# Kernel optimization log

Measured on AMD Instinct MI355X. Metric: run time of the kernel, lower is better.

The kernel has to match this reference:

```python
import jax, jax.numpy as jnp
import numpy as np


def conv3x3_reflect(x, w):
    # x: [B,C,H,W], w: [O,I,3,3]; reflect pad 1, stride 1, no bias
    xp = jnp.pad(x, ((0, 0), (0, 0), (1, 1), (1, 1)), mode='reflect')
    return jax.lax.conv_general_dilated(
        xp, w, window_strides=(1, 1), padding='VALID',
        dimension_numbers=('NCHW', 'OIHW', 'NCHW'))


def prelu(x, alpha):
    return jnp.where(x >= 0, x, alpha * x)


def nonlocal_block(x, wg, wth, wph, wW):
    # x: [B,C,H,W]; all weights [O,C] (1x1 convs, no bias)
    B, C, H, W = x.shape
    xf = x.reshape(B, C, H * W)                     # [B,C,N]
    g_x = jnp.einsum('oc,bcn->bno', wg, xf)         # [B,N,Ci]
    theta_x = jnp.einsum('oc,bcn->bno', wth, xf)    # [B,N,Ci]
    phi_x = jnp.einsum('oc,bcn->bon', wph, xf)      # [B,Ci,N]
    f = jnp.einsum('bic,bcj->bij', theta_x, phi_x)  # [B,N,N]
    # NOTE: original code softmaxes over dim=1 (rows), not the last dim
    f_div_C = jax.nn.softmax(f, axis=1)
    y = jnp.einsum('bij,bjc->bic', f_div_C, g_x)    # [B,N,Ci]
    y = y.transpose(0, 2, 1).reshape(B, -1, H, W)   # [B,Ci,H,W]
    W_y = jnp.einsum('oc,bchw->bohw', wW, y)
    return W_y + x


def setup_inputs() -> dict:
    key = jax.random.key(0)
    ks = jax.random.split(key, 8)
    B, C, H, W = 2, 64, 80, 80
    s33 = 1.0 / np.sqrt(C * 9)
    s11 = 1.0 / np.sqrt(C)
    return {
        'x': jax.random.normal(ks[0], (B, C, H, W), jnp.float32),
        'w1': jax.random.normal(ks[1], (C, C, 3, 3), jnp.float32) * s33,
        'w2': jax.random.normal(ks[2], (C, C, 3, 3), jnp.float32) * s33,
        'wg': jax.random.normal(ks[3], (C, C), jnp.float32) * s11,
        'wth': jax.random.normal(ks[4], (C, C), jnp.float32) * s11,
        'wph': jax.random.normal(ks[5], (C, C), jnp.float32) * s11,
        'wW': jax.random.normal(ks[6], (C, C), jnp.float32) * s11,
        'alpha': jnp.asarray(0.25, jnp.float32),
    }


def reference(x, w1, w2, wg, wth, wph, wW, alpha):
    x1 = conv3x3_reflect(x, w1)          # conv1; becomes residual source
    out = prelu(x1, alpha)
    out = nonlocal_block(out, wg, wth, wph, wW)
    out = out + x1                       # out += x (x was rebound to conv1 output)
    out = conv3x3_reflect(out, w2)       # conv2 (BasicConv, relu=False, bn=None)
    out = prelu(out, alpha)
    return out
```

## Files before the change

kernel.cpp:

```cpp
#include <hip/hip_runtime.h>
#include <hip/hip_bf16.h>
#include <cstddef>


constexpr int kB = 2, kC = 64, kH = 80, kW = 80, kN = kH * kW;
constexpr int kSJ = 10, kChunk = kN / kSJ, kNT = kChunk / 64;
constexpr float kLOG2E = 1.4426950408889634f;

typedef __attribute__((ext_vector_type(8))) short short8;
typedef __attribute__((ext_vector_type(4))) float f32x4;

__device__ __forceinline__ uint pkbf(float a, float b) {
  union { __hip_bfloat162 h; uint u; } x;
  x.h.x = __float2bfloat16(a);
  x.h.y = __float2bfloat16(b);
  return x.u;
}

__device__ __forceinline__ uint pktr(float a, float b) {
  return __builtin_amdgcn_perm(__float_as_uint(b), __float_as_uint(a),
                               0x07060302u);
}

#define GL16(gsrc, ldst)                                                    \
  __builtin_amdgcn_global_load_lds(                                         \
      (__attribute__((address_space(1))) void*)(char*)(gsrc),               \
      (__attribute__((address_space(3))) void*)(ldst), 16, 0, 0)

__global__ void k_prep(const float* __restrict__ w1, const float* __restrict__ w2,
                       const float* __restrict__ wth, const float* __restrict__ wph,
                       const float* __restrict__ wg, const float* __restrict__ wWm,
                       ushort* __restrict__ wc1, ushort* __restrict__ wc2,
                       __hip_bfloat16* __restrict__ Mb,
                       __hip_bfloat16* __restrict__ wgb,
                       __hip_bfloat16* __restrict__ wWb) {
  const int idx = blockIdx.x * 256 + threadIdx.x;
  {
    const int o = idx / (kC * 9);
    const int r = idx % (kC * 9);
    const int ci = r / 9, tap = r % 9;
    const int og = o >> 4, il = o & 15;
    const int kc = ci >> 5, hi = (ci >> 3) & 3, e = ci & 7;
    const int pos = ((tap * 2 + kc) * 4 + og) * 512 + (hi * 16 + il) * 8 + e;
    union { __hip_bfloat16 h; ushort u; } c1, c2;
    c1.h = __float2bfloat16(w1[idx]);
    c2.h = __float2bfloat16(w2[idx]);
    wc1[pos] = c1.u;
    wc2[pos] = c2.u;
  }
  if (idx < kC * kC) {
    const int a = idx >> 6, bb = idx & 63;
    float s = 0.f;
    for (int o = 0; o < kC; ++o) s += wth[o * kC + a] * wph[o * kC + bb];
    Mb[idx] = __float2bfloat16(s * kLOG2E);
    wgb[idx] = __float2bfloat16(wg[idx]);
    wWb[idx] = __float2bfloat16(wWm[idx]);
  }
}

__global__ __launch_bounds__(256) void k_tobf(const float* __restrict__ x,
                                              ushort* __restrict__ xb) {
  const int b = blockIdx.y;
  const int j0 = blockIdx.x * 64;
  const int t = threadIdx.x;
  __shared__ ushort tile[64][68];
  {
    const int c = t >> 2, jseg = (t & 3) * 16;
    const float* s = &x[((size_t)b * kC + c) * kN + j0 + jseg];
#pragma unroll
    for (int k = 0; k < 16; ++k) {
      union { __hip_bfloat16 h; ushort u; } cv;
      cv.h = __float2bfloat16(s[k]);
      tile[c][jseg + k] = cv.u;
    }
  }
  __syncthreads();
  {
    const int j = t >> 2, cseg = (t & 3) * 16;
    union { short8 v; ushort u[8]; } o0, o1;
#pragma unroll
    for (int k = 0; k < 16; ++k) {
      const ushort u = tile[cseg + k][j];
      if (k < 8) o0.u[k] = u; else o1.u[k - 8] = u;
    }
    short8* d = (short8*)&xb[((size_t)b * kN + j0 + j) * kC + cseg];
    d[0] = o0.v;
    d[1] = o1.v;
  }
}

template <int MODE>
__global__ __launch_bounds__(256) void k_convm(
    const ushort* __restrict__ xb, const ushort* __restrict__ wc,
    const float* __restrict__ alphap, float* __restrict__ raw,
    ushort* __restrict__ pt, const __hip_bfloat16* __restrict__ Mb,
    const __hip_bfloat16* __restrict__ wgb, __hip_bfloat16* __restrict__ phb,
    __hip_bfloat16* __restrict__ gb) {
  const int tile = blockIdx.x;
  const int b = blockIdx.y;
  const int r0 = tile / 5, c0 = (tile % 5) * 16;
  const int lane = threadIdx.x & 63, w = threadIdx.x >> 6;
  const int il = lane & 15, hi = lane >> 4;

  __shared__ ushort zt[16][72];

  short8 wt[9][2];
#pragma unroll
  for (int t = 0; t < 9; ++t)
#pragma unroll
    for (int kc = 0; kc < 2; ++kc)
      wt[t][kc] = *(const short8*)&wc[(size_t)((t * 2 + kc) * 4 + w) * 512 + lane * 8];

  int cl[3], rb[3];
#pragma unroll
  for (int d = 0; d < 3; ++d) {
    const int cc = c0 + il + d - 1;
    cl[d] = cc < 0 ? 1 : (cc > kW - 1 ? kW - 2 : cc);
    const int rr = r0 + d - 1;
    rb[d] = rr < 0 ? 1 : (rr > kH - 1 ? kH - 2 : rr);
  }
  const ushort* xB = xb + (size_t)b * kN * kC;

  f32x4 acc = {0.f, 0.f, 0.f, 0.f};
#pragma unroll
  for (int dh = 0; dh < 3; ++dh) {
    const int nb = rb[dh] * kW;
#pragma unroll
    for (int dw = 0; dw < 3; ++dw) {
      const ushort* src = &xB[(size_t)(nb + cl[dw]) * kC + hi * 8];
      const short8 a0 = *(const short8*)src;
      const short8 a1 = *(const short8*)(src + 32);
      acc = __builtin_amdgcn_mfma_f32_16x16x32_bf16(a0, wt[dh * 3 + dw][0], acc, 0, 0, 0);
      acc = __builtin_amdgcn_mfma_f32_16x16x32_bf16(a1, wt[dh * 3 + dw][1], acc, 0, 0, 0);
    }
  }

  const int n0 = r0 * kW + c0;
  const float alpha = alphap[0];
  if (MODE == 0) {
    *(f32x4*)&raw[((size_t)b * kC + w * 16 + il) * kN + n0 + hi * 4] = acc;
#pragma unroll
    for (int r = 0; r < 4; ++r) {
      const float v = acc[r];
      union { __hip_bfloat16 h; ushort u; } cv;
      cv.h = __float2bfloat16(v >= 0.f ? v : alpha * v);
      zt[hi * 4 + r][w * 16 + il] = cv.u;
    }
    __syncthreads();
    {
      const int t = threadIdx.x;
      const int px = t >> 4, cb = (t & 15) * 4;
      uint2 o2;
      o2.x = (uint)zt[px][cb] | ((uint)zt[px][cb + 1] << 16);
      o2.y = (uint)zt[px][cb + 2] | ((uint)zt[px][cb + 3] << 16);
      *(uint2*)&pt[((size_t)b * kN + n0 + px) * kC + cb] = o2;
    }
    {
      const int n = n0 + il;
      const short8 b0 = *(const short8*)&zt[il][hi * 8];
      const short8 b1 = *(const short8*)&zt[il][32 + hi * 8];
      const short8 am0 = *(const short8*)&Mb[(size_t)(w * 16 + il) * kC + hi * 8];
      const short8 am1 = *(const short8*)&Mb[(size_t)(w * 16 + il) * kC + 32 + hi * 8];
      f32x4 o4 = {0.f, 0.f, 0.f, 0.f};
      o4 = __builtin_amdgcn_mfma_f32_16x16x32_bf16(am0, b0, o4, 0, 0, 0);
      o4 = __builtin_amdgcn_mfma_f32_16x16x32_bf16(am1, b1, o4, 0, 0, 0);
      uint2 p2;
      p2.x = pkbf(o4[0], o4[1]);
      p2.y = pkbf(o4[2], o4[3]);
      *(uint2*)&phb[((size_t)b * kN + n) * kC + w * 16 + hi * 4] = p2;
      const short8 ag0 = *(const short8*)&wgb[(size_t)(w * 16 + il) * kC + hi * 8];
      const short8 ag1 = *(const short8*)&wgb[(size_t)(w * 16 + il) * kC + 32 + hi * 8];
      f32x4 g4 = {0.f, 0.f, 0.f, 0.f};
      g4 = __builtin_amdgcn_mfma_f32_16x16x32_bf16(ag0, b0, g4, 0, 0, 0);
      g4 = __builtin_amdgcn_mfma_f32_16x16x32_bf16(ag1, b1, g4, 0, 0, 0);
      uint2 g2;
      g2.x = pkbf(g4[0], g4[1]);
      g2.y = pkbf(g4[2], g4[3]);
      *(uint2*)&gb[((size_t)b * kN + n) * kC + w * 16 + hi * 4] = g2;
    }
  } else {
    f32x4 pr;
#pragma unroll
    for (int r = 0; r < 4; ++r) {
      const float v = acc[r];
      pr[r] = v >= 0.f ? v : alpha * v;
    }
    *(f32x4*)&raw[((size_t)b * kC + w * 16 + il) * kN + n0 + hi * 4] = pr;
  }
}

__global__ __launch_bounds__(256, 2) void k_colstat(
    const __hip_bfloat16* __restrict__ th, const __hip_bfloat16* __restrict__ ph,
    float* __restrict__ partial) {
  const int b = blockIdx.z, ic = blockIdx.y;
  const int lane = threadIdx.x & 63, w = threadIdx.x >> 6;
  const int il = lane & 15, hi = lane >> 4;
  const int j0w = blockIdx.x * 128 + w * 32;

  __shared__ __align__(16) ushort tbufA[8192], tbufB[8192];

  const __hip_bfloat16* thB = th + (size_t)b * kN * kC;
  const size_t phr0 = ((size_t)b * kN + j0w + il) * kC;
  const size_t phr1 = ((size_t)b * kN + j0w + 16 + il) * kC;
  const short8 a00 = *(const short8*)&ph[phr0 + hi * 8];
  const short8 a01 = *(const short8*)&ph[phr0 + 32 + hi * 8];
  const short8 a10 = *(const short8*)&ph[phr1 + hi * 8];
  const short8 a11 = *(const short8*)&ph[phr1 + 32 + hi * 8];

  const int f0 = 2 * w;
  const char* st[2];
#pragma unroll
  for (int k = 0; k < 2; ++k) {
    const int f = f0 + k;
    st[k] = (const char*)&thB[(size_t)(ic * kChunk + (f >> 1) * 16 + il) * kC +
                              (f & 1) * 32 + hi * 8];
  }

#define CSTAGE1(DST)                                                        \
  {                                                                         \
    _Pragma("unroll") for (int k = 0; k < 2; ++k) {                         \
      GL16(st[k], &(DST)[(f0 + k) * 512]);                                  \
      st[k] += (size_t)64 * kC * 2;                                         \
    }                                                                       \
  }
#define CSTAGE2(DST) { CSTAGE1(DST) CSTAGE1((DST) + 4096) }

#define CCOMP1(SRC)                                                        \
  {                                                                        \
    const ushort* bp_ = SRC;                                               \
    _Pragma("unroll") for (int s = 0; s < 4; ++s) {                        \
      const short8 bf0 = *(const short8*)&bp_[(2 * s) * 512 + lane * 8];   \
      const short8 bf1 = *(const short8*)&bp_[(2 * s + 1) * 512 + lane * 8];\
      f32x4 sj0 = {0.f, 0.f, 0.f, 0.f};                                    \
      f32x4 sj1 = {0.f, 0.f, 0.f, 0.f};                                    \
      sj0 = __builtin_amdgcn_mfma_f32_16x16x32_bf16(a00, bf0, sj0, 0, 0, 0);\
      sj0 = __builtin_amdgcn_mfma_f32_16x16x32_bf16(a01, bf1, sj0, 0, 0, 0);\
      sj1 = __builtin_amdgcn_mfma_f32_16x16x32_bf16(a10, bf0, sj1, 0, 0, 0);\
      sj1 = __builtin_amdgcn_mfma_f32_16x16x32_bf16(a11, bf1, sj1, 0, 0, 0);\
      _Pragma("unroll") for (int r = 0; r < 4; ++r) {                      \
        cs0[r] += exp2f(sj0[r]);                                           \
        cs1[r] += exp2f(sj1[r]);                                           \
      }                                                                    \
    }                                                                      \
  }
#define CCOMP2(SRC) { CCOMP1(SRC) CCOMP1((SRC) + 4096) }

  float cs0[4] = {0.f, 0.f, 0.f, 0.f};
  float cs1[4] = {0.f, 0.f, 0.f, 0.f};
  CSTAGE2(tbufA);
  __syncthreads();
#pragma unroll 1
  for (int t = 0; t < 2; ++t) {
    CSTAGE2(tbufB);
    CCOMP2(tbufA);
    __syncthreads();
    CSTAGE2(tbufA);
    CCOMP2(tbufB);
    __syncthreads();
  }
  CCOMP2(tbufA);
#undef CSTAGE1
#undef CSTAGE2
#undef CCOMP1
#undef CCOMP2

#pragma unroll
  for (int r = 0; r < 4; ++r) {
    cs0[r] += __shfl_xor(cs0[r], 1); cs1[r] += __shfl_xor(cs1[r], 1);
    cs0[r] += __shfl_xor(cs0[r], 2); cs1[r] += __shfl_xor(cs1[r], 2);
    cs0[r] += __shfl_xor(cs0[r], 4); cs1[r] += __shfl_xor(cs1[r], 4);
    cs0[r] += __shfl_xor(cs0[r], 8); cs1[r] += __shfl_xor(cs1[r], 8);
  }
  if (il == 0) {
    float* p = partial + (size_t)(b * kSJ + ic) * kN + j0w + hi * 4;
#pragma unroll
    for (int r = 0; r < 4; ++r) {
      p[r] = cs0[r];
      p[16 + r] = cs1[r];
    }
  }
}

__global__ __launch_bounds__(256) void k_gscale(
    const __hip_bfloat16* __restrict__ gb, const float* __restrict__ partial,
    __hip_bfloat16* __restrict__ gT) {
  const int b = blockIdx.y;
  const int j0 = blockIdx.x * 64;
  const int t = threadIdx.x;
  __shared__ ushort tile[64][66];
  __shared__ float rsv[64];
  if (t < 64) {
    const int j = j0 + t;
    float cs = 0.f;
#pragma unroll
    for (int s = 0; s < kSJ; ++s) cs += partial[(size_t)(b * kSJ + s) * kN + j];
    rsv[t] = 1.0f / cs;
  }
  {
    const int jl = t >> 2, cseg = (t & 3) * 16;
    const ushort* src = (const ushort*)&gb[((size_t)b * kN + j0 + jl) * kC + cseg];
    union { short8 v; ushort u[8]; } u0, u1;
    u0.v = *(const short8*)src;
    u1.v = *(const short8*)(src + 8);
#pragma unroll
    for (int k = 0; k < 8; ++k) {
      tile[jl][cseg + k] = u0.u[k];
      tile[jl][cseg + 8 + k] = u1.u[k];
    }
  }
  __syncthreads();
  const int c = t >> 2, jseg = (t & 3) * 16;
  union { short8 v; ushort u[8]; } o0, o1;
#pragma unroll
  for (int k = 0; k < 16; ++k) {
    const int j = jseg + k;
    const float gv = __uint_as_float((uint)tile[j][c] << 16);
    union { __hip_bfloat16 h; ushort us; } cv;
    cv.h = __float2bfloat16(gv * rsv[j]);
    if (k < 8) o0.u[k] = cv.us; else o1.u[k - 8] = cv.us;
  }
  short8* dst = (short8*)&gT[((size_t)b * kC + c) * kN + j0 + jseg];
  dst[0] = o0.v;
  dst[1] = o1.v;
}

__global__ __launch_bounds__(256, 2) void k_nl(
    const __hip_bfloat16* __restrict__ th, const __hip_bfloat16* __restrict__ ph,
    const __hip_bfloat16* __restrict__ gT, ushort* __restrict__ py) {
  const int js = blockIdx.y, b = blockIdx.z;
  const int lane = threadIdx.x & 63, w = threadIdx.x >> 6;
  const int il = lane & 15, hi = lane >> 4;
  const int itile32 = blockIdx.x * 4 + w;
  const int i0w = itile32 * 32;
  const int jstart = js * kChunk;
  const int jbase = ((il >> 2) << 3) + (il & 3);

  __shared__ __align__(16) ushort bufA[16384], bufB[16384];

  const __hip_bfloat16* phB = ph + (size_t)b * kN * kC;
  const __hip_bfloat16* gTB = gT + (size_t)b * kC * kN;

  const size_t tr0 = ((size_t)b * kN + i0w + il) * kC;
  const size_t tr1 = ((size_t)b * kN + i0w + 16 + il) * kC;
  const short8 tA0k0 = *(const short8*)&th[tr0 + hi * 8];
  const short8 tA0k1 = *(const short8*)&th[tr0 + 32 + hi * 8];
  const short8 tA1k0 = *(const short8*)&th[tr1 + hi * 8];
  const short8 tA1k1 = *(const short8*)&th[tr1 + 32 + hi * 8];

  const int f0 = 2 * w;
  const char* sp[2];
  const char* sg[2];
#pragma unroll
  for (int k = 0; k < 2; ++k) {
    const int f = f0 + k;
    const int pr = jstart + jbase + ((f >> 1) & 1) * 4 + ((f >> 2) & 1) * 32;
    const int pc = (f & 1) * 32 + hi * 8;
    sp[k] = (const char*)&phB[(size_t)pr * kC + pc];
    const int gc = (f & 3) * 16 + il;
    const int gj = jstart + ((f >> 2) & 1) * 32 + hi * 8;
    sg[k] = (const char*)&gTB[(size_t)gc * kN + gj];
  }

#define NLSTAGE1(DST)                                                       \
  {                                                                         \
    _Pragma("unroll") for (int k = 0; k < 2; ++k) {                         \
      GL16(sp[k], &(DST)[(f0 + k) * 512]);                                  \
      GL16(sg[k], &(DST)[4096 + (f0 + k) * 512]);                           \
      sp[k] += (size_t)64 * kC * 2;                                         \
      sg[k] += (size_t)64 * 2;                                              \
    }                                                                       \
  }
#define NLSTAGE2(DST) { NLSTAGE1(DST) NLSTAGE1((DST) + 8192) }

#define QKI(TB0, TB1, s0, s1, s2, s3)                                        \
    f32x4 s0 = {0.f, 0.f, 0.f, 0.f};                                         \
    f32x4 s1 = {0.f, 0.f, 0.f, 0.f};                                         \
    f32x4 s2 = {0.f, 0.f, 0.f, 0.f};                                         \
    f32x4 s3 = {0.f, 0.f, 0.f, 0.f};                                         \
    s0 = __builtin_amdgcn_mfma_f32_16x16x32_bf16(pa0, TB0, s0, 0, 0, 0);     \
    s0 = __builtin_amdgcn_mfma_f32_16x16x32_bf16(pa1, TB1, s0, 0, 0, 0);     \
    s1 = __builtin_amdgcn_mfma_f32_16x16x32_bf16(pa2, TB0, s1, 0, 0, 0);     \
    s1 = __builtin_amdgcn_mfma_f32_16x16x32_bf16(pa3, TB1, s1, 0, 0, 0);     \
    s2 = __builtin_amdgcn_mfma_f32_16x16x32_bf16(pa4, TB0, s2, 0, 0, 0);     \
    s2 = __builtin_amdgcn_mfma_f32_16x16x32_bf16(pa5, TB1, s2, 0, 0, 0);     \
    s3 = __builtin_amdgcn_mfma_f32_16x16x32_bf16(pa6, TB0, s3, 0, 0, 0);     \
    s3 = __builtin_amdgcn_mfma_f32_16x16x32_bf16(pa7, TB1, s3, 0, 0, 0);

#define PACK2(sa, sb, pb)                                                    \
    short8 pb;                                                               \
    {                                                                        \
      uint* pw_ = (uint*)&pb;                                                \
      pw_[0] = pktr(exp2f(sa[0]), exp2f(sa[1]));                             \
      pw_[1] = pktr(exp2f(sa[2]), exp2f(sa[3]));                             \
      pw_[2] = pktr(exp2f(sb[0]), exp2f(sb[1]));                             \
      pw_[3] = pktr(exp2f(sb[2]), exp2f(sb[3]));                             \
    }

#define NLCOMP1(SRC)                                                         \
  {                                                                          \
    const ushort* bp_ = SRC;                                                 \
    const short8 pa0 = *(const short8*)&bp_[0 * 512 + lane * 8];             \
    const short8 pa1 = *(const short8*)&bp_[1 * 512 + lane * 8];             \
    const short8 pa2 = *(const short8*)&bp_[2 * 512 + lane * 8];             \
    const short8 pa3 = *(const short8*)&bp_[3 * 512 + lane * 8];             \
    const short8 pa4 = *(const short8*)&bp_[4 * 512 + lane * 8];             \
    const short8 pa5 = *(const short8*)&bp_[5 * 512 + lane * 8];             \
    const short8 pa6 = *(const short8*)&bp_[6 * 512 + lane * 8];             \
    const short8 pa7 = *(const short8*)&bp_[7 * 512 + lane * 8];             \
    const short8 ga0 = *(const short8*)&bp_[4096 + 0 * 512 + lane * 8];      \
    const short8 ga1 = *(const short8*)&bp_[4096 + 1 * 512 + lane * 8];      \
    const short8 ga2 = *(const short8*)&bp_[4096 + 2 * 512 + lane * 8];      \
    const short8 ga3 = *(const short8*)&bp_[4096 + 3 * 512 + lane * 8];      \
    const short8 ga4 = *(const short8*)&bp_[4096 + 4 * 512 + lane * 8];      \
    const short8 ga5 = *(const short8*)&bp_[4096 + 5 * 512 + lane * 8];      \
    const short8 ga6 = *(const short8*)&bp_[4096 + 6 * 512 + lane * 8];      \
    const short8 ga7 = *(const short8*)&bp_[4096 + 7 * 512 + lane * 8];      \
    {                                                                        \
      QKI(tA0k0, tA0k1, s00, s01, s02, s03)                                  \
      PACK2(s00, s01, pb00)                                                  \
      PACK2(s02, s03, pb01)                                                  \
      ay00 = __builtin_amdgcn_mfma_f32_16x16x32_bf16(ga0, pb00, ay00, 0, 0, 0);\
      ay01 = __builtin_amdgcn_mfma_f32_16x16x32_bf16(ga1, pb00, ay01, 0, 0, 0);\
      ay02 = __builtin_amdgcn_mfma_f32_16x16x32_bf16(ga2, pb00, ay02, 0, 0, 0);\
      ay03 = __builtin_amdgcn_mfma_f32_16x16x32_bf16(ga3, pb00, ay03, 0, 0, 0);\
      ay00 = __builtin_amdgcn_mfma_f32_16x16x32_bf16(ga4, pb01, ay00, 0, 0, 0);\
      ay01 = __builtin_amdgcn_mfma_f32_16x16x32_bf16(ga5, pb01, ay01, 0, 0, 0);\
      ay02 = __builtin_amdgcn_mfma_f32_16x16x32_bf16(ga6, pb01, ay02, 0, 0, 0);\
      ay03 = __builtin_amdgcn_mfma_f32_16x16x32_bf16(ga7, pb01, ay03, 0, 0, 0);\
    }                                                                        \
    {                                                                        \
      QKI(tA1k0, tA1k1, s10, s11, s12, s13)                                  \
      PACK2(s10, s11, pb10)                                                  \
      PACK2(s12, s13, pb11)                                                  \
      ay10 = __builtin_amdgcn_mfma_f32_16x16x32_bf16(ga0, pb10, ay10, 0, 0, 0);\
      ay11 = __builtin_amdgcn_mfma_f32_16x16x32_bf16(ga1, pb10, ay11, 0, 0, 0);\
      ay12 = __builtin_amdgcn_mfma_f32_16x16x32_bf16(ga2, pb10, ay12, 0, 0, 0);\
      ay13 = __builtin_amdgcn_mfma_f32_16x16x32_bf16(ga3, pb10, ay13, 0, 0, 0);\
      ay10 = __builtin_amdgcn_mfma_f32_16x16x32_bf16(ga4, pb11, ay10, 0, 0, 0);\
      ay11 = __builtin_amdgcn_mfma_f32_16x16x32_bf16(ga5, pb11, ay11, 0, 0, 0);\
      ay12 = __builtin_amdgcn_mfma_f32_16x16x32_bf16(ga6, pb11, ay12, 0, 0, 0);\
      ay13 = __builtin_amdgcn_mfma_f32_16x16x32_bf16(ga7, pb11, ay13, 0, 0, 0);\
    }                                                                        \
  }
#define NLCOMP2(SRC) { NLCOMP1(SRC) NLCOMP1((SRC) + 8192) }

  f32x4 ay00 = {0.f, 0.f, 0.f, 0.f}, ay01 = {0.f, 0.f, 0.f, 0.f};
  f32x4 ay02 = {0.f, 0.f, 0.f, 0.f}, ay03 = {0.f, 0.f, 0.f, 0.f};
  f32x4 ay10 = {0.f, 0.f, 0.f, 0.f}, ay11 = {0.f, 0.f, 0.f, 0.f};
  f32x4 ay12 = {0.f, 0.f, 0.f, 0.f}, ay13 = {0.f, 0.f, 0.f, 0.f};

  NLSTAGE2(bufA);
  __syncthreads();
#pragma unroll 1
  for (int t = 0; t < 2; ++t) {
    NLSTAGE2(bufB);
    NLCOMP2(bufA);
    __syncthreads();
    NLSTAGE2(bufA);
    NLCOMP2(bufB);
    __syncthreads();
  }
  NLCOMP2(bufA);
#undef NLSTAGE1
#undef NLSTAGE2
#undef NLCOMP1
#undef NLCOMP2
#undef QKI
#undef PACK2

  uint* b32 = (uint*)(py + ((size_t)(js * kB + b) * (kN / 32) + itile32) * 2048);
  b32[0 * 64 + lane] = pkbf(ay00[0], ay00[1]);
  b32[1 * 64 + lane] = pkbf(ay00[2], ay00[3]);
  b32[2 * 64 + lane] = pkbf(ay01[0], ay01[1]);
  b32[3 * 64 + lane] = pkbf(ay01[2], ay01[3]);
  b32[4 * 64 + lane] = pkbf(ay02[0], ay02[1]);
  b32[5 * 64 + lane] = pkbf(ay02[2], ay02[3]);
  b32[6 * 64 + lane] = pkbf(ay03[0], ay03[1]);
  b32[7 * 64 + lane] = pkbf(ay03[2], ay03[3]);
  b32[8 * 64 + lane] = pkbf(ay10[0], ay10[1]);
  b32[9 * 64 + lane] = pkbf(ay10[2], ay10[3]);
  b32[10 * 64 + lane] = pkbf(ay11[0], ay11[1]);
  b32[11 * 64 + lane] = pkbf(ay11[2], ay11[3]);
  b32[12 * 64 + lane] = pkbf(ay12[0], ay12[1]);
  b32[13 * 64 + lane] = pkbf(ay12[2], ay12[3]);
  b32[14 * 64 + lane] = pkbf(ay13[0], ay13[1]);
  b32[15 * 64 + lane] = pkbf(ay13[2], ay13[3]);
}

__global__ __launch_bounds__(128) void k_wy(
    const ushort* __restrict__ py, const __hip_bfloat16* __restrict__ wWb,
    const float* __restrict__ x1, const float* __restrict__ alphap,
    ushort* __restrict__ zb) {
  const int b = blockIdx.y;
  const int lane = threadIdx.x & 63, w = threadIdx.x >> 6;
  const int il = lane & 15, hi = lane >> 4;
  const int itile32 = blockIdx.x * 2 + w;
  const int i0w = itile32 * 32;

  __shared__ __align__(16) ushort yt2[2][32 * 72];
  __shared__ __align__(16) ushort zt2[2][32 * 72];
  ushort* yt = yt2[w];
  ushort* zt = zt2[w];

  float lo[16], hs[16];
#pragma unroll
  for (int k = 0; k < 16; ++k) { lo[k] = 0.f; hs[k] = 0.f; }
#pragma unroll 1
  for (int s = 0; s < kSJ; ++s) {
    const uint* ps =
        (const uint*)(py + ((size_t)(s * kB + b) * (kN / 32) + itile32) * 2048);
#pragma unroll
    for (int k = 0; k < 16; ++k) {
      const uint u = ps[k * 64 + lane];
      lo[k] += __uint_as_float(u << 16);
      hs[k] += __uint_as_float(u & 0xffff0000u);
    }
  }
#pragma unroll
  for (int k = 0; k < 16; ++k) {
    const int row = (k >> 3) * 16 + il;
    const int col = ((k >> 1) & 3) * 16 + hi * 4 + (k & 1) * 2;
    *(uint*)&yt[row * 72 + col] = pkbf(lo[k], hs[k]);
  }

  const float alpha = alphap[0];
#pragma unroll
  for (int a = 0; a < 2; ++a) {
    const short8 by0 = *(const short8*)&yt[(a * 16 + il) * 72 + hi * 8];
    const short8 by1 = *(const short8*)&yt[(a * 16 + il) * 72 + 32 + hi * 8];
#pragma unroll
    for (int q = 0; q < 4; ++q) {
      const short8 af0 = *(const short8*)&wWb[(size_t)(q * 16 + il) * kC + hi * 8];
      const short8 af1 = *(const short8*)&wWb[(size_t)(q * 16 + il) * kC + 32 + hi * 8];
      f32x4 o4 = {0.f, 0.f, 0.f, 0.f};
      o4 = __builtin_amdgcn_mfma_f32_16x16x32_bf16(af0, by0, o4, 0, 0, 0);
      o4 = __builtin_amdgcn_mfma_f32_16x16x32_bf16(af1, by1, o4, 0, 0, 0);
      float zv[4];
#pragma unroll
      for (int r = 0; r < 4; ++r) {
        const int o = q * 16 + hi * 4 + r;
        const size_t idx = ((size_t)b * kC + o) * kN + i0w + a * 16 + il;
        const float xv = x1[idx];
        const float pr = xv >= 0.f ? xv : alpha * xv;
        zv[r] = o4[r] + pr + xv;
      }
      *(uint*)&zt[(a * 16 + il) * 72 + q * 16 + hi * 4] = pkbf(zv[0], zv[1]);
      *(uint*)&zt[(a * 16 + il) * 72 + q * 16 + hi * 4 + 2] = pkbf(zv[2], zv[3]);
    }
  }

  const int px = lane >> 1, cseg = (lane & 1) * 32;
  short8* d = (short8*)&zb[((size_t)b * kN + i0w + px) * kC + cseg];
#pragma unroll
  for (int k = 0; k < 4; ++k)
    d[k] = *(const short8*)&zt[px * 72 + cseg + k * 8];
}

extern "C" void kernel_launch(void* const* d_in, const int* in_sizes, int n_in,
                              void* d_out, int out_size, void* d_ws, size_t ws_size,
                              hipStream_t stream) {
  const float* x      = (const float*)d_in[0];
  const float* w1     = (const float*)d_in[1];
  const float* w2     = (const float*)d_in[2];
  const float* wg     = (const float*)d_in[3];
  const float* wth    = (const float*)d_in[4];
  const float* wph    = (const float*)d_in[5];
  const float* wWm    = (const float*)d_in[6];
  const float* alphap = (const float*)d_in[7];
  float* out = (float*)d_out;

  const size_t SZ = (size_t)kB * kC * kN;

  float* x1 = (float*)d_ws;
  __hip_bfloat16* pTb = (__hip_bfloat16*)(x1 + SZ);
  __hip_bfloat16* phb = pTb + SZ;
  __hip_bfloat16* gb  = phb + SZ;
  __hip_bfloat16* gT  = gb + SZ;
  float* partial = (float*)(gT + SZ);
  ushort* wc1 = (ushort*)(partial + (size_t)kB * kSJ * kN);
  ushort* wc2 = wc1 + 9 * kC * kC;
  __hip_bfloat16* Mb  = (__hip_bfloat16*)(wc2 + 9 * kC * kC);
  __hip_bfloat16* wgb = Mb + kC * kC;
  __hip_bfloat16* wWb = wgb + kC * kC;
  ushort* py = (ushort*)(wWb + kC * kC);
  ushort* xb = py;
  ushort* zb = (ushort*)gb;

  k_prep<<<144, 256, 0, stream>>>(w1, w2, wth, wph, wg, wWm, wc1, wc2,
                                  Mb, wgb, wWb);
  k_tobf<<<dim3(kN / 64, kB), 256, 0, stream>>>(x, xb);
  k_convm<0><<<dim3(400, kB), 256, 0, stream>>>(xb, wc1, alphap, x1,
                                                (ushort*)pTb, Mb, wgb, phb, gb);
  k_colstat<<<dim3(kN / 128, kSJ, kB), 256, 0, stream>>>(pTb, phb, partial);
  k_gscale<<<dim3(kN / 64, kB), 256, 0, stream>>>(gb, partial, gT);
  k_nl<<<dim3(kN / 128, kSJ, kB), 256, 0, stream>>>(pTb, phb, gT, py);
  k_wy<<<dim3(kN / 64, kB), 128, 0, stream>>>(py, wWb, x1, alphap, zb);
  k_convm<1><<<dim3(400, kB), 256, 0, stream>>>(zb, wc2, alphap, out, nullptr,
                                                nullptr, nullptr, nullptr,
                                                nullptr);
}
```

Measured before the change: 109.1 us.

## Widen per-wave row tiles to 64 in colstat/nl and merge tobf into prep

Each wave in k_colstat and k_nl now handles 64 query/key rows instead of 32, so every staged LDS tile of theta/phi/g is reused across twice as many MFMA rows. This halves the grid and halves the LDS and global staging traffic per unit of work, but raises per-wave register use (16 accumulators in k_nl). The py partial layout is changed to 64-row tiles and k_wy indexing is updated to match. Separately, the bf16 conversion of x is merged into k_prep as extra blocks, which removes one kernel launch.

```diff
diff --git a/kernel.cpp b/kernel.cpp
--- a/kernel.cpp
+++ b/kernel.cpp
@@ -27,41 +27,43 @@
       (__attribute__((address_space(1))) void*)(char*)(gsrc),               \
       (__attribute__((address_space(3))) void*)(ldst), 16, 0, 0)
 
-__global__ void k_prep(const float* __restrict__ w1, const float* __restrict__ w2,
-                       const float* __restrict__ wth, const float* __restrict__ wph,
-                       const float* __restrict__ wg, const float* __restrict__ wWm,
-                       ushort* __restrict__ wc1, ushort* __restrict__ wc2,
-                       __hip_bfloat16* __restrict__ Mb,
-                       __hip_bfloat16* __restrict__ wgb,
-                       __hip_bfloat16* __restrict__ wWb) {
-  const int idx = blockIdx.x * 256 + threadIdx.x;
-  {
-    const int o = idx / (kC * 9);
-    const int r = idx % (kC * 9);
-    const int ci = r / 9, tap = r % 9;
-    const int og = o >> 4, il = o & 15;
-    const int kc = ci >> 5, hi = (ci >> 3) & 3, e = ci & 7;
-    const int pos = ((tap * 2 + kc) * 4 + og) * 512 + (hi * 16 + il) * 8 + e;
-    union { __hip_bfloat16 h; ushort u; } c1, c2;
-    c1.h = __float2bfloat16(w1[idx]);
-    c2.h = __float2bfloat16(w2[idx]);
-    wc1[pos] = c1.u;
-    wc2[pos] = c2.u;
-  }
-  if (idx < kC * kC) {
-    const int a = idx >> 6, bb = idx & 63;
-    float s = 0.f;
-    for (int o = 0; o < kC; ++o) s += wth[o * kC + a] * wph[o * kC + bb];
-    Mb[idx] = __float2bfloat16(s * kLOG2E);
-    wgb[idx] = __float2bfloat16(wg[idx]);
-    wWb[idx] = __float2bfloat16(wWm[idx]);
-  }
-}
-
-__global__ __launch_bounds__(256) void k_tobf(const float* __restrict__ x,
-                                              ushort* __restrict__ xb) {
-  const int b = blockIdx.y;
-  const int j0 = blockIdx.x * 64;
+__global__ __launch_bounds__(256) void k_prep(
+    const float* __restrict__ w1, const float* __restrict__ w2,
+    const float* __restrict__ wth, const float* __restrict__ wph,
+    const float* __restrict__ wg, const float* __restrict__ wWm,
+    const float* __restrict__ x, ushort* __restrict__ wc1,
+    ushort* __restrict__ wc2, __hip_bfloat16* __restrict__ Mb,
+    __hip_bfloat16* __restrict__ wgb, __hip_bfloat16* __restrict__ wWb,
+    ushort* __restrict__ xb) {
+  const int bx = blockIdx.x;
+  if (bx < 144) {
+    const int idx = bx * 256 + threadIdx.x;
+    {
+      const int o = idx / (kC * 9);
+      const int r = idx % (kC * 9);
+      const int ci = r / 9, tap = r % 9;
+      const int og = o >> 4, il = o & 15;
+      const int kc = ci >> 5, hi = (ci >> 3) & 3, e = ci & 7;
+      const int pos = ((tap * 2 + kc) * 4 + og) * 512 + (hi * 16 + il) * 8 + e;
+      union { __hip_bfloat16 h; ushort u; } c1, c2;
+      c1.h = __float2bfloat16(w1[idx]);
+      c2.h = __float2bfloat16(w2[idx]);
+      wc1[pos] = c1.u;
+      wc2[pos] = c2.u;
+    }
+    if (idx < kC * kC) {
+      const int a = idx >> 6, bb = idx & 63;
+      float s = 0.f;
+      for (int o = 0; o < kC; ++o) s += wth[o * kC + a] * wph[o * kC + bb];
+      Mb[idx] = __float2bfloat16(s * kLOG2E);
+      wgb[idx] = __float2bfloat16(wg[idx]);
+      wWb[idx] = __float2bfloat16(wWm[idx]);
+    }
+    return;
+  }
+  const int tb = bx - 144;
+  const int b = tb / 100;
+  const int j0 = (tb % 100) * 64;
   const int t = threadIdx.x;
   __shared__ ushort tile[64][68];
   {
@@ -195,17 +197,18 @@
   const int b = blockIdx.z, ic = blockIdx.y;
   const int lane = threadIdx.x & 63, w = threadIdx.x >> 6;
   const int il = lane & 15, hi = lane >> 4;
-  const int j0w = blockIdx.x * 128 + w * 32;
+  const int j0w = blockIdx.x * 256 + w * 64;
 
   __shared__ __align__(16) ushort tbufA[8192], tbufB[8192];
 
   const __hip_bfloat16* thB = th + (size_t)b * kN * kC;
-  const size_t phr0 = ((size_t)b * kN + j0w + il) * kC;
-  const size_t phr1 = ((size_t)b * kN + j0w + 16 + il) * kC;
-  const short8 a00 = *(const short8*)&ph[phr0 + hi * 8];
-  const short8 a01 = *(const short8*)&ph[phr0 + 32 + hi * 8];
-  const short8 a10 = *(const short8*)&ph[phr1 + hi * 8];
-  const short8 a11 = *(const short8*)&ph[phr1 + 32 + hi * 8];
+  short8 aA[4][2];
+#pragma unroll
+  for (int c = 0; c < 4; ++c) {
+    const size_t pr = ((size_t)b * kN + j0w + c * 16 + il) * kC;
+    aA[c][0] = *(const short8*)&ph[pr + hi * 8];
+    aA[c][1] = *(const short8*)&ph[pr + 32 + hi * 8];
+  }
 
   const int f0 = 2 * w;
   const char* st[2];
@@ -231,22 +234,23 @@
     _Pragma("unroll") for (int s = 0; s < 4; ++s) {                        \
       const short8 bf0 = *(const short8*)&bp_[(2 * s) * 512 + lane * 8];   \
       const short8 bf1 = *(const short8*)&bp_[(2 * s + 1) * 512 + lane * 8];\
-      f32x4 sj0 = {0.f, 0.f, 0.f, 0.f};                                    \
-      f32x4 sj1 = {0.f, 0.f, 0.f, 0.f};                                    \
-      sj0 = __builtin_amdgcn_mfma_f32_16x16x32_bf16(a00, bf0, sj0, 0, 0, 0);\
-      sj0 = __builtin_amdgcn_mfma_f32_16x16x32_bf16(a01, bf1, sj0, 0, 0, 0);\
-      sj1 = __builtin_amdgcn_mfma_f32_16x16x32_bf16(a10, bf0, sj1, 0, 0, 0);\
-      sj1 = __builtin_amdgcn_mfma_f32_16x16x32_bf16(a11, bf1, sj1, 0, 0, 0);\
-      _Pragma("unroll") for (int r = 0; r < 4; ++r) {                      \
-        cs0[r] += exp2f(sj0[r]);                                           \
-        cs1[r] += exp2f(sj1[r]);                                           \
+      _Pragma("unroll") for (int c = 0; c < 4; ++c) {                      \
+        f32x4 sj = {0.f, 0.f, 0.f, 0.f};                                   \
+        sj = __builtin_amdgcn_mfma_f32_16x16x32_bf16(aA[c][0], bf0, sj, 0, 0, 0);\
+        sj = __builtin_amdgcn_mfma_f32_16x16x32_bf16(aA[c][1], bf1, sj, 0, 0, 0);\
+        _Pragma("unroll") for (int r = 0; r < 4; ++r)                      \
+            cs[c][r] += exp2f(sj[r]);                                      \
       }                                                                    \
     }                                                                      \
   }
 #define CCOMP2(SRC) { CCOMP1(SRC) CCOMP1((SRC) + 4096) }
 
-  float cs0[4] = {0.f, 0.f, 0.f, 0.f};
-  float cs1[4] = {0.f, 0.f, 0.f, 0.f};
+  float cs[4][4];
+#pragma unroll
+  for (int c = 0; c < 4; ++c)
+#pragma unroll
+    for (int r = 0; r < 4; ++r) cs[c][r] = 0.f;
+
   CSTAGE2(tbufA);
   __syncthreads();
 #pragma unroll 1
@@ -265,19 +269,20 @@
 #undef CCOMP2
 
 #pragma unroll
-  for (int r = 0; r < 4; ++r) {
-    cs0[r] += __shfl_xor(cs0[r], 1); cs1[r] += __shfl_xor(cs1[r], 1);
-    cs0[r] += __shfl_xor(cs0[r], 2); cs1[r] += __shfl_xor(cs1[r], 2);
-    cs0[r] += __shfl_xor(cs0[r], 4); cs1[r] += __shfl_xor(cs1[r], 4);
-    cs0[r] += __shfl_xor(cs0[r], 8); cs1[r] += __shfl_xor(cs1[r], 8);
-  }
+  for (int c = 0; c < 4; ++c)
+#pragma unroll
+    for (int r = 0; r < 4; ++r) {
+      cs[c][r] += __shfl_xor(cs[c][r], 1);
+      cs[c][r] += __shfl_xor(cs[c][r], 2);
+      cs[c][r] += __shfl_xor(cs[c][r], 4);
+      cs[c][r] += __shfl_xor(cs[c][r], 8);
+    }
   if (il == 0) {
     float* p = partial + (size_t)(b * kSJ + ic) * kN + j0w + hi * 4;
 #pragma unroll
-    for (int r = 0; r < 4; ++r) {
-      p[r] = cs0[r];
-      p[16 + r] = cs1[r];
-    }
+    for (int c = 0; c < 4; ++c)
+#pragma unroll
+      for (int r = 0; r < 4; ++r) p[c * 16 + r] = cs[c][r];
   }
 }
 
@@ -330,8 +335,8 @@
   const int js = blockIdx.y, b = blockIdx.z;
   const int lane = threadIdx.x & 63, w = threadIdx.x >> 6;
   const int il = lane & 15, hi = lane >> 4;
-  const int itile32 = blockIdx.x * 4 + w;
-  const int i0w = itile32 * 32;
+  const int itile64 = blockIdx.x * 4 + w;
+  const int i0w = itile64 * 64;
   const int jstart = js * kChunk;
   const int jbase = ((il >> 2) << 3) + (il & 3);
 
@@ -340,12 +345,13 @@
   const __hip_bfloat16* phB = ph + (size_t)b * kN * kC;
   const __hip_bfloat16* gTB = gT + (size_t)b * kC * kN;
 
-  const size_t tr0 = ((size_t)b * kN + i0w + il) * kC;
-  const size_t tr1 = ((size_t)b * kN + i0w + 16 + il) * kC;
-  const short8 tA0k0 = *(const short8*)&th[tr0 + hi * 8];
-  const short8 tA0k1 = *(const short8*)&th[tr0 + 32 + hi * 8];
-  const short8 tA1k0 = *(const short8*)&th[tr1 + hi * 8];
-  const short8 tA1k1 = *(const short8*)&th[tr1 + 32 + hi * 8];
+  short8 tA[4][2];
+#pragma unroll
+  for (int c = 0; c < 4; ++c) {
+    const size_t tr = ((size_t)b * kN + i0w + c * 16 + il) * kC;
+    tA[c][0] = *(const short8*)&th[tr + hi * 8];
+    tA[c][1] = *(const short8*)&th[tr + 32 + hi * 8];
+  }
 
   const int f0 = 2 * w;
   const char* sp[2];
@@ -372,82 +378,50 @@
   }
 #define NLSTAGE2(DST) { NLSTAGE1(DST) NLSTAGE1((DST) + 8192) }
 
-#define QKI(TB0, TB1, s0, s1, s2, s3)                                        \
-    f32x4 s0 = {0.f, 0.f, 0.f, 0.f};                                         \
-    f32x4 s1 = {0.f, 0.f, 0.f, 0.f};                                         \
-    f32x4 s2 = {0.f, 0.f, 0.f, 0.f};                                         \
-    f32x4 s3 = {0.f, 0.f, 0.f, 0.f};                                         \
-    s0 = __builtin_amdgcn_mfma_f32_16x16x32_bf16(pa0, TB0, s0, 0, 0, 0);     \
-    s0 = __builtin_amdgcn_mfma_f32_16x16x32_bf16(pa1, TB1, s0, 0, 0, 0);     \
-    s1 = __builtin_amdgcn_mfma_f32_16x16x32_bf16(pa2, TB0, s1, 0, 0, 0);     \
-    s1 = __builtin_amdgcn_mfma_f32_16x16x32_bf16(pa3, TB1, s1, 0, 0, 0);     \
-    s2 = __builtin_amdgcn_mfma_f32_16x16x32_bf16(pa4, TB0, s2, 0, 0, 0);     \
-    s2 = __builtin_amdgcn_mfma_f32_16x16x32_bf16(pa5, TB1, s2, 0, 0, 0);     \
-    s3 = __builtin_amdgcn_mfma_f32_16x16x32_bf16(pa6, TB0, s3, 0, 0, 0);     \
-    s3 = __builtin_amdgcn_mfma_f32_16x16x32_bf16(pa7, TB1, s3, 0, 0, 0);
-
-#define PACK2(sa, sb, pb)                                                    \
-    short8 pb;                                                               \
-    {                                                                        \
-      uint* pw_ = (uint*)&pb;                                                \
-      pw_[0] = pktr(exp2f(sa[0]), exp2f(sa[1]));                             \
-      pw_[1] = pktr(exp2f(sa[2]), exp2f(sa[3]));                             \
-      pw_[2] = pktr(exp2f(sb[0]), exp2f(sb[1]));                             \
-      pw_[3] = pktr(exp2f(sb[2]), exp2f(sb[3]));                             \
-    }
-
 #define NLCOMP1(SRC)                                                         \
   {                                                                          \
     const ushort* bp_ = SRC;                                                 \
-    const short8 pa0 = *(const short8*)&bp_[0 * 512 + lane * 8];             \
-    const short8 pa1 = *(const short8*)&bp_[1 * 512 + lane * 8];             \
-    const short8 pa2 = *(const short8*)&bp_[2 * 512 + lane * 8];             \
-    const short8 pa3 = *(const short8*)&bp_[3 * 512 + lane * 8];             \
-    const short8 pa4 = *(const short8*)&bp_[4 * 512 + lane * 8];             \
-    const short8 pa5 = *(const short8*)&bp_[5 * 512 + lane * 8];             \
-    const short8 pa6 = *(const short8*)&bp_[6 * 512 + lane * 8];             \
-    const short8 pa7 = *(const short8*)&bp_[7 * 512 + lane * 8];             \
-    const short8 ga0 = *(const short8*)&bp_[4096 + 0 * 512 + lane * 8];      \
-    const short8 ga1 = *(const short8*)&bp_[4096 + 1 * 512 + lane * 8];      \
-    const short8 ga2 = *(const short8*)&bp_[4096 + 2 * 512 + lane * 8];      \
-    const short8 ga3 = *(const short8*)&bp_[4096 + 3 * 512 + lane * 8];      \
-    const short8 ga4 = *(const short8*)&bp_[4096 + 4 * 512 + lane * 8];      \
-    const short8 ga5 = *(const short8*)&bp_[4096 + 5 * 512 + lane * 8];      \
-    const short8 ga6 = *(const short8*)&bp_[4096 + 6 * 512 + lane * 8];      \
-    const short8 ga7 = *(const short8*)&bp_[4096 + 7 * 512 + lane * 8];      \
-    {                                                                        \
-      QKI(tA0k0, tA0k1, s00, s01, s02, s03)                                  \
-      PACK2(s00, s01, pb00)                                                  \
-      PACK2(s02, s03, pb01)                                                  \
-      ay00 = __builtin_amdgcn_mfma_f32_16x16x32_bf16(ga0, pb00, ay00, 0, 0, 0);\
-      ay01 = __builtin_amdgcn_mfma_f32_16x16x32_bf16(ga1, pb00, ay01, 0, 0, 0);\
-      ay02 = __builtin_amdgcn_mfma_f32_16x16x32_bf16(ga2, pb00, ay02, 0, 0, 0);\
-      ay03 = __builtin_amdgcn_mfma_f32_16x16x32_bf16(ga3, pb00, ay03, 0, 0, 0);\
-      ay00 = __builtin_amdgcn_mfma_f32_16x16x32_bf16(ga4, pb01, ay00, 0, 0, 0);\
-      ay01 = __builtin_amdgcn_mfma_f32_16x16x32_bf16(ga5, pb01, ay01, 0, 0, 0);\
-      ay02 = __builtin_amdgcn_mfma_f32_16x16x32_bf16(ga6, pb01, ay02, 0, 0, 0);\
-      ay03 = __builtin_amdgcn_mfma_f32_16x16x32_bf16(ga7, pb01, ay03, 0, 0, 0);\
+    short8 pa[8], ga[8];                                                     \
+    _Pragma("unroll") for (int f = 0; f < 8; ++f) {                          \
+      pa[f] = *(const short8*)&bp_[f * 512 + lane * 8];                      \
+      ga[f] = *(const short8*)&bp_[4096 + f * 512 + lane * 8];               \
     }                                                                        \
-    {                                                                        \
-      QKI(tA1k0, tA1k1, s10, s11, s12, s13)                                  \
-      PACK2(s10, s11, pb10)                                                  \
-      PACK2(s12, s13, pb11)                                                  \
-      ay10 = __builtin_amdgcn_mfma_f32_16x16x32_bf16(ga0, pb10, ay10, 0, 0, 0);\
-      ay11 = __builtin_amdgcn_mfma_f32_16x16x32_bf16(ga1, pb10, ay11, 0, 0, 0);\
-      ay12 = __builtin_amdgcn_mfma_f32_16x16x32_bf16(ga2, pb10, ay12, 0, 0, 0);\
-      ay13 = __builtin_amdgcn_mfma_f32_16x16x32_bf16(ga3, pb10, ay13, 0, 0, 0);\
-      ay10 = __builtin_amdgcn_mfma_f32_16x16x32_bf16(ga4, pb11, ay10, 0, 0, 0);\
-      ay11 = __builtin_amdgcn_mfma_f32_16x16x32_bf16(ga5, pb11, ay11, 0, 0, 0);\
-      ay12 = __builtin_amdgcn_mfma_f32_16x16x32_bf16(ga6, pb11, ay12, 0, 0, 0);\
-      ay13 = __builtin_amdgcn_mfma_f32_16x16x32_bf16(ga7, pb11, ay13, 0, 0, 0);\
+    _Pragma("unroll") for (int c = 0; c < 4; ++c) {                          \
+      f32x4 s[4];                                                            \
+      _Pragma("unroll") for (int q = 0; q < 4; ++q) {                        \
+        f32x4 z = {0.f, 0.f, 0.f, 0.f};                                     \
+        z = __builtin_amdgcn_mfma_f32_16x16x32_bf16(pa[2 * q], tA[c][0], z, 0, 0, 0); \
+        z = __builtin_amdgcn_mfma_f32_16x16x32_bf16(pa[2 * q + 1], tA[c][1], z, 0, 0, 0); \
+        s[q] = z;                                                            \
+      }                                                                      \
+      short8 pb0, pb1;                                                       \
+      {                                                                      \
+        uint* pw_ = (uint*)&pb0;                                             \
+        pw_[0] = pktr(exp2f(s[0][0]), exp2f(s[0][1]));                       \
+        pw_[1] = pktr(exp2f(s[0][2]), exp2f(s[0][3]));                       \
+        pw_[2] = pktr(exp2f(s[1][0]), exp2f(s[1][1]));                       \
+        pw_[3] = pktr(exp2f(s[1][2]), exp2f(s[1][3]));                       \
+      }                                                                      \
+      {                                                                      \
+        uint* pw_ = (uint*)&pb1;                                             \
+        pw_[0] = pktr(exp2f(s[2][0]), exp2f(s[2][1]));                       \
+        pw_[1] = pktr(exp2f(s[2][2]), exp2f(s[2][3]));                       \
+        pw_[2] = pktr(exp2f(s[3][0]), exp2f(s[3][1]));                       \
+        pw_[3] = pktr(exp2f(s[3][2]), exp2f(s[3][3]));                       \
+      }                                                                      \
+      _Pragma("unroll") for (int q = 0; q < 4; ++q)                          \
+          ay[c][q] = __builtin_amdgcn_mfma_f32_16x16x32_bf16(ga[q], pb0, ay[c][q], 0, 0, 0); \
+      _Pragma("unroll") for (int q = 0; q < 4; ++q)                          \
+          ay[c][q] = __builtin_amdgcn_mfma_f32_16x16x32_bf16(ga[4 + q], pb1, ay[c][q], 0, 0, 0); \
     }                                                                        \
   }
 #define NLCOMP2(SRC) { NLCOMP1(SRC) NLCOMP1((SRC) + 8192) }
 
-  f32x4 ay00 = {0.f, 0.f, 0.f, 0.f}, ay01 = {0.f, 0.f, 0.f, 0.f};
-  f32x4 ay02 = {0.f, 0.f, 0.f, 0.f}, ay03 = {0.f, 0.f, 0.f, 0.f};
-  f32x4 ay10 = {0.f, 0.f, 0.f, 0.f}, ay11 = {0.f, 0.f, 0.f, 0.f};
-  f32x4 ay12 = {0.f, 0.f, 0.f, 0.f}, ay13 = {0.f, 0.f, 0.f, 0.f};
+  f32x4 ay[4][4];
+#pragma unroll
+  for (int c = 0; c < 4; ++c)
+#pragma unroll
+    for (int q = 0; q < 4; ++q) ay[c][q] = {0.f, 0.f, 0.f, 0.f};
 
   NLSTAGE2(bufA);
   __syncthreads();
@@ -465,26 +439,15 @@
 #undef NLSTAGE2
 #undef NLCOMP1
 #undef NLCOMP2
-#undef QKI
-#undef PACK2
-
-  uint* b32 = (uint*)(py + ((size_t)(js * kB + b) * (kN / 32) + itile32) * 2048);
-  b32[0 * 64 + lane] = pkbf(ay00[0], ay00[1]);
-  b32[1 * 64 + lane] = pkbf(ay00[2], ay00[3]);
-  b32[2 * 64 + lane] = pkbf(ay01[0], ay01[1]);
-  b32[3 * 64 + lane] = pkbf(ay01[2], ay01[3]);
-  b32[4 * 64 + lane] = pkbf(ay02[0], ay02[1]);
-  b32[5 * 64 + lane] = pkbf(ay02[2], ay02[3]);
-  b32[6 * 64 + lane] = pkbf(ay03[0], ay03[1]);
-  b32[7 * 64 + lane] = pkbf(ay03[2], ay03[3]);
-  b32[8 * 64 + lane] = pkbf(ay10[0], ay10[1]);
-  b32[9 * 64 + lane] = pkbf(ay10[2], ay10[3]);
-  b32[10 * 64 + lane] = pkbf(ay11[0], ay11[1]);
-  b32[11 * 64 + lane] = pkbf(ay11[2], ay11[3]);
-  b32[12 * 64 + lane] = pkbf(ay12[0], ay12[1]);
-  b32[13 * 64 + lane] = pkbf(ay12[2], ay12[3]);
-  b32[14 * 64 + lane] = pkbf(ay13[0], ay13[1]);
-  b32[15 * 64 + lane] = pkbf(ay13[2], ay13[3]);
+
+  uint* b32 = (uint*)(py + ((size_t)(js * kB + b) * (kN / 64) + itile64) * 4096);
+#pragma unroll
+  for (int c = 0; c < 4; ++c)
+#pragma unroll
+    for (int q = 0; q < 4; ++q) {
+      b32[(c * 8 + q * 2 + 0) * 64 + lane] = pkbf(ay[c][q][0], ay[c][q][1]);
+      b32[(c * 8 + q * 2 + 1) * 64 + lane] = pkbf(ay[c][q][2], ay[c][q][3]);
+    }
 }
 
 __global__ __launch_bounds__(128) void k_wy(
@@ -496,6 +459,7 @@
   const int il = lane & 15, hi = lane >> 4;
   const int itile32 = blockIdx.x * 2 + w;
   const int i0w = itile32 * 32;
+  const int itile64 = itile32 >> 1, half = itile32 & 1;
 
   __shared__ __align__(16) ushort yt2[2][32 * 72];
   __shared__ __align__(16) ushort zt2[2][32 * 72];
@@ -508,7 +472,9 @@
 #pragma unroll 1
   for (int s = 0; s < kSJ; ++s) {
     const uint* ps =
-        (const uint*)(py + ((size_t)(s * kB + b) * (kN / 32) + itile32) * 2048);
+        (const uint*)(py +
+                      ((size_t)(s * kB + b) * (kN / 64) + itile64) * 4096) +
+        half * 1024;
 #pragma unroll
     for (int k = 0; k < 16; ++k) {
       const uint u = ps[k * 64 + lane];
@@ -586,14 +552,13 @@
   ushort* xb = py;
   ushort* zb = (ushort*)gb;
 
-  k_prep<<<144, 256, 0, stream>>>(w1, w2, wth, wph, wg, wWm, wc1, wc2,
-                                  Mb, wgb, wWb);
-  k_tobf<<<dim3(kN / 64, kB), 256, 0, stream>>>(x, xb);
+  k_prep<<<344, 256, 0, stream>>>(w1, w2, wth, wph, wg, wWm, x,
+                                  wc1, wc2, Mb, wgb, wWb, xb);
   k_convm<0><<<dim3(400, kB), 256, 0, stream>>>(xb, wc1, alphap, x1,
                                                 (ushort*)pTb, Mb, wgb, phb, gb);
-  k_colstat<<<dim3(kN / 128, kSJ, kB), 256, 0, stream>>>(pTb, phb, partial);
+  k_colstat<<<dim3(kN / 256, kSJ, kB), 256, 0, stream>>>(pTb, phb, partial);
   k_gscale<<<dim3(kN / 64, kB), 256, 0, stream>>>(gb, partial, gT);
-  k_nl<<<dim3(kN / 128, kSJ, kB), 256, 0, stream>>>(pTb, phb, gT, py);
+  k_nl<<<dim3(kN / 256, kSJ, kB), 256, 0, stream>>>(pTb, phb, gT, py);
   k_wy<<<dim3(kN / 64, kB), 128, 0, stream>>>(py, wWb, x1, alphap, zb);
   k_convm<1><<<dim3(400, kB), 256, 0, stream>>>(zb, wc2, alphap, out, nullptr,
                                                 nullptr, nullptr, nullptr,
```

After: 106.1 us. 1.03x faster.
